# Kernel tuning notes

Measured on AMD Instinct MI355X. Metric: run time of the kernel, lower is better.

Reference implementation:

```python
import jax, jax.numpy as jnp
import numpy as np

ALPHA = 0.2  # LeakyReLU negative slope
NEG_INF = -9.0e15


def setup_inputs() -> dict:
    key = jax.random.key(0)
    k1, k2, k3, k4 = jax.random.split(key, 4)
    B, T, N, Fin, Fout = 2, 8, 2048, 64, 64
    h = jax.random.normal(k1, (B, T, N, Fin), dtype=jnp.float32)
    # xavier_uniform-like init for W [Fin,Fout] and a [2*Fout,1]
    limW = 1.414 * np.sqrt(6.0 / (Fin + Fout))
    W = jax.random.uniform(k2, (Fin, Fout), minval=-limW, maxval=limW, dtype=jnp.float32)
    lima = 1.414 * np.sqrt(6.0 / (2 * Fout + 1))
    a = jax.random.uniform(k3, (2 * Fout, 1), minval=-lima, maxval=lima, dtype=jnp.float32)
    adj = jax.random.randint(k4, (N, N), 0, 2).astype(jnp.int32)
    return {"h": h, "W": W, "a": a, "adj": adj}


def reference(h, W, a, adj):
    Fout = W.shape[1]
    Wh = jnp.matmul(h, W)                      # [B,T,N,Fout]
    Wh1 = jnp.matmul(Wh, a[:Fout])             # [B,T,N,1]
    Wh2 = jnp.matmul(Wh, a[Fout:])             # [B,T,N,1]
    e = Wh1 + jnp.swapaxes(Wh2, -1, -2)        # [B,T,N,N]
    e = jnp.where(e > 0, e, ALPHA * e)         # LeakyReLU
    e = jnp.where(adj > 0, e, jnp.float32(NEG_INF))  # adjacency mask
    # NOTE: source does F.softmax(dim=1) -> softmax over the T axis, replicated faithfully
    attention = jax.nn.softmax(e, axis=1)
    # dropout omitted (eval-mode reference)
    out = jnp.matmul(attention, Wh)            # [B,T,N,Fout]
    return jax.nn.elu(out)                     # concat=True
```

## Files before the change

### kernel.cpp

```cpp
#include <hip/hip_runtime.h>
#include <math.h>

#define B_ 2
#define T_ 8
#define N_ 2048
#define F_ 64
#define TI 32
#define JC 64
#define JCP 72
#define LOG2E 1.44269504088896f
#define PART_STRIDE ((size_t)B_ * T_ * N_ * F_)

typedef __attribute__((ext_vector_type(8))) short short8;
typedef __attribute__((ext_vector_type(4))) float f32x4;

__device__ __forceinline__ unsigned short f2bf(float x) {
  unsigned u = __float_as_uint(x);
  u += 0x7FFFu + ((u >> 16) & 1u);
  return (unsigned short)(u >> 16);
}

__device__ __forceinline__ unsigned cvt_pk_bf16(float lo, float hi) {
  unsigned r;
  asm("v_cvt_pk_bf16_f32 %0, %1, %2" : "=v"(r) : "v"(lo), "v"(hi));
  return r;
}

__global__ __launch_bounds__(256) void prep_kernel(
    const float* __restrict__ h, const float* __restrict__ W,
    const float* __restrict__ a, unsigned short* __restrict__ WhT,
    float* __restrict__ Wh1, float* __restrict__ Wh2) {
  __shared__ float Ws[64][64];
  __shared__ float hs[64][64];
  __shared__ float Whs[64][65];
  const int tid = threadIdx.x;
  const int row0 = blockIdx.x * 64;
  const int bt = row0 >> 11;
  const int j0 = row0 & 2047;
  for (int i = tid; i < 4096; i += 256) Ws[i >> 6][i & 63] = W[i];
  for (int i = tid; i < 4096; i += 256) hs[i >> 6][i & 63] = h[(size_t)row0 * 64 + i];
  __syncthreads();
  const int f = tid & 63;
  const int rq = tid >> 6;
  float acc[16];
#pragma unroll
  for (int m = 0; m < 16; ++m) acc[m] = 0.f;
#pragma unroll 4
  for (int k = 0; k < 64; ++k) {
    const float wvv = Ws[k][f];
#pragma unroll
    for (int m = 0; m < 16; ++m) acc[m] = fmaf(hs[rq * 16 + m][k], wvv, acc[m]);
  }
#pragma unroll
  for (int m = 0; m < 16; ++m) Whs[rq * 16 + m][f] = acc[m];
  __syncthreads();
  {
    const int r = tid >> 2, q = tid & 3;
    float s1 = 0.f, s2 = 0.f;
#pragma unroll
    for (int k = 0; k < 16; ++k) {
      const float v = Whs[r][q * 16 + k];
      s1 = fmaf(v, a[q * 16 + k], s1);
      s2 = fmaf(v, a[64 + q * 16 + k], s2);
    }
    s1 += __shfl_xor(s1, 1); s1 += __shfl_xor(s1, 2);
    s2 += __shfl_xor(s2, 1); s2 += __shfl_xor(s2, 2);
    if (q == 0) {
      Wh1[(size_t)bt * N_ + j0 + r] = s1 * LOG2E;
      Wh2[(size_t)bt * N_ + j0 + r] = s2 * LOG2E;
    }
  }
  {
    const int ff = tid & 63, cp = tid >> 6;
#pragma unroll
    for (int cc = 0; cc < 2; ++cc) {
      const int c = cp * 2 + cc;
      short8 v;
#pragma unroll
      for (int k = 0; k < 8; ++k) v[k] = (short)f2bf(Whs[c * 8 + k][ff]);
      *(short8*)(WhT + ((size_t)bt * 64 + ff) * N_ + j0 + c * 8) = v;
    }
  }
}

__global__ __launch_bounds__(512, 4) void gat_mfma(
    const unsigned short* __restrict__ WhT, const float* __restrict__ Wh1,
    const float* __restrict__ Wh2, const int* __restrict__ adj,
    float* __restrict__ out, float* __restrict__ parts, const int njq) {
  __shared__ unsigned short atts[2][T_][TI][JCP];
  __shared__ float wh2s[2][T_][JC];
  const int tid = threadIdx.x;
  const int jq = blockIdx.x % njq;
  const int rest = blockIdx.x / njq;
  const int i0 = (rest & 63) * TI;
  const int b = rest >> 6;
  const int jspan = N_ / njq;
  const int jbase = jq * jspan;
  const int nchunk = jspan / JC;

  const int wv = tid >> 6;
  const int lane = tid & 63;
  const int col = lane & 15;
  const int kg = lane >> 4;

  const int sii = tid >> 4;
  const int sjj = (tid & 15) * 4;
  const int st = tid >> 6, sj = tid & 63;

  const unsigned short* wtb = WhT + (size_t)(b * T_ + wv) * F_ * N_;
  const float* wh2b = Wh2 + (size_t)b * T_ * N_;
  const int* adjrow = adj + (size_t)(i0 + sii) * N_ + jbase;

  float w1r[T_];
#pragma unroll
  for (int t = 0; t < T_; ++t) w1r[t] = Wh1[(size_t)(b * T_ + t) * N_ + i0 + sii];

  f32x4 acc[2][4];
#pragma unroll
  for (int it = 0; it < 2; ++it)
#pragma unroll
    for (int nt = 0; nt < 4; ++nt) acc[it][nt] = {0.f, 0.f, 0.f, 0.f};

  wh2s[0][st][sj] = wh2b[(size_t)st * N_ + jbase + sj];
  int4 ad = *(const int4*)(adjrow + sjj);
  __syncthreads();

  for (int c = 0; c < nchunk; ++c) {
    const int j0 = jbase + c * JC;
    const int buf = c & 1;
    short8 breg[4][2];
#pragma unroll
    for (int nt = 0; nt < 4; ++nt)
#pragma unroll
      for (int ks = 0; ks < 2; ++ks)
        breg[nt][ks] = *(const short8*)(wtb + (size_t)(nt * 16 + col) * N_ +
                                        j0 + ks * 32 + kg * 8);
    if (c + 1 < nchunk)
      wh2s[buf ^ 1][st][sj] = wh2b[(size_t)st * N_ + j0 + JC + sj];
    int4 adn = ad;
    if (c + 1 < nchunk) adn = *(const int4*)(adjrow + (c + 1) * JC + sjj);

#pragma unroll
    for (int g = 0; g < 2; ++g) {
      const int c0 = sjj + 2 * g;
      const int a0i = g == 0 ? ad.x : ad.z;
      const int a1i = g == 0 ? ad.y : ad.w;
      float e0[T_], e1[T_];
      float s0 = 0.f, s1 = 0.f;
#pragma unroll
      for (int t = 0; t < T_; ++t) {
        const float2 w2 = *(const float2*)(&wh2s[buf][t][c0]);
        float x0 = w1r[t] + w2.x;
        float x1 = w1r[t] + w2.y;
        x0 = fmaxf(x0, 0.2f * x0);
        x1 = fmaxf(x1, 0.2f * x1);
        e0[t] = __builtin_amdgcn_exp2f(x0);
        e1[t] = __builtin_amdgcn_exp2f(x1);
        s0 += e0[t];
        s1 += e1[t];
      }
      const float r0 = a0i > 0 ? __builtin_amdgcn_rcpf(s0) : 0.f;
      const float r1 = a1i > 0 ? __builtin_amdgcn_rcpf(s1) : 0.f;
      const float d0 = a0i > 0 ? 0.f : 0.125f;
      const float d1 = a1i > 0 ? 0.f : 0.125f;
#pragma unroll
      for (int t = 0; t < T_; ++t) {
        const float av0 = fmaf(e0[t], r0, d0);
        const float av1 = fmaf(e1[t], r1, d1);
        *(unsigned*)&atts[buf][t][sii][c0] = cvt_pk_bf16(av0, av1);
      }
    }
    ad = adn;
    __syncthreads();
#pragma unroll
    for (int it = 0; it < 2; ++it) {
      const unsigned short* ab = &atts[buf][wv][it * 16 + col][kg * 8];
      const short8 a0 = *(const short8*)ab;
      const short8 a1 = *(const short8*)(ab + 32);
#pragma unroll
      for (int nt = 0; nt < 4; ++nt) {
        acc[it][nt] = __builtin_amdgcn_mfma_f32_16x16x32_bf16(a0, breg[nt][0], acc[it][nt], 0, 0, 0);
        acc[it][nt] = __builtin_amdgcn_mfma_f32_16x16x32_bf16(a1, breg[nt][1], acc[it][nt], 0, 0, 0);
      }
    }
  }

  float* dst = (jq == 0) ? out : (parts + (size_t)(jq - 1) * PART_STRIDE);
  float* ob = dst + ((size_t)(b * T_ + wv) * N_ + i0) * F_;
#pragma unroll
  for (int it = 0; it < 2; ++it) {
#pragma unroll
    for (int nt = 0; nt < 4; ++nt) {
#pragma unroll
      for (int r = 0; r < 4; ++r) {
        const int row = it * 16 + kg * 4 + r;
        ob[(size_t)row * F_ + nt * 16 + col] = acc[it][nt][r];
      }
    }
  }
}

__global__ __launch_bounds__(256) void combine_elu(
    float* __restrict__ out, const float* __restrict__ parts, const int nparts) {
  const size_t i = ((size_t)blockIdx.x * 256 + threadIdx.x) * 4;
  f32x4 o = *(const f32x4*)(out + i);
  for (int p = 0; p < nparts; ++p) {
    const f32x4 q = *(const f32x4*)(parts + p * PART_STRIDE + i);
#pragma unroll
    for (int k = 0; k < 4; ++k) o[k] += q[k];
  }
#pragma unroll
  for (int k = 0; k < 4; ++k) o[k] = o[k] > 0.f ? o[k] : expm1f(o[k]);
  *(f32x4*)(out + i) = o;
}

extern "C" void kernel_launch(void* const* d_in, const int* in_sizes, int n_in,
                              void* d_out, int out_size, void* d_ws, size_t ws_size,
                              hipStream_t stream) {
  const float* h   = (const float*)d_in[0];
  const float* W   = (const float*)d_in[1];
  const float* a   = (const float*)d_in[2];
  const int*   adj = (const int*)d_in[3];
  float* out = (float*)d_out;

  const size_t whtBytes = (size_t)B_ * T_ * F_ * N_ * 2;
  const size_t vBytes   = (size_t)B_ * T_ * N_ * 4;
  const size_t partB    = PART_STRIDE * 4;

  unsigned short* WhT = (unsigned short*)d_ws;
  float* Wh1   = (float*)((char*)d_ws + whtBytes);
  float* Wh2   = Wh1 + (size_t)B_ * T_ * N_;
  float* parts = Wh2 + (size_t)B_ * T_ * N_;

  const int njq = (ws_size >= whtBytes + 2 * vBytes + 3 * partB) ? 4
                : (ws_size >= whtBytes + 2 * vBytes + 1 * partB) ? 2 : 1;

  hipLaunchKernelGGL(prep_kernel, dim3(B_ * T_ * N_ / 64), dim3(256), 0, stream,
                     h, W, a, WhT, Wh1, Wh2);
  hipLaunchKernelGGL(gat_mfma, dim3(B_ * 64 * njq), dim3(512), 0, stream,
                     WhT, Wh1, Wh2, adj, out, parts, njq);
  if (njq > 1) {
    hipLaunchKernelGGL(combine_elu, dim3((unsigned)(PART_STRIDE / (256 * 4))), dim3(256),
                       0, stream, out, parts, njq - 1);
  } else {
    hipLaunchKernelGGL(combine_elu, dim3((unsigned)(PART_STRIDE / (256 * 4))), dim3(256),
                       0, stream, out, parts, 0);
  }
}
```

Measured before the change: 62.64 us.

## Store split-K partials in bf16, raise split to eight, add priority and lightweight barriers

The attention kernel now writes every split-K partial as bf16 into the workspace, and the combine kernel sums all partials and applies ELU with 8-wide vector loads. The split factor grows from 4 to 8 when the workspace allows, giving more blocks to fill the GPU. Barriers are replaced by an explicit lgkmcnt wait plus s_barrier, and the MFMA section runs at raised wave priority. The aim is to cut partial-sum write traffic and improve occupancy, at the cost of bf16 rounding in the partials, extra partial traffic from the larger split, and one more combine input per element.

```diff
diff --git a/kernel.cpp b/kernel.cpp
--- a/kernel.cpp
+++ b/kernel.cpp
@@ -25,6 +25,16 @@
   asm("v_cvt_pk_bf16_f32 %0, %1, %2" : "=v"(r) : "v"(lo), "v"(hi));
   return r;
 }
+
+__device__ __forceinline__ float bf2f(unsigned short u) {
+  return __uint_as_float(((unsigned)u) << 16);
+}
+
+#define BARRIER() do {                                      \
+    asm volatile("s_waitcnt lgkmcnt(0)" ::: "memory");      \
+    __builtin_amdgcn_s_barrier();                           \
+    __builtin_amdgcn_sched_barrier(0);                      \
+  } while (0)
 
 __global__ __launch_bounds__(256) void prep_kernel(
     const float* __restrict__ h, const float* __restrict__ W,
@@ -86,7 +96,7 @@
 __global__ __launch_bounds__(512, 4) void gat_mfma(
     const unsigned short* __restrict__ WhT, const float* __restrict__ Wh1,
     const float* __restrict__ Wh2, const int* __restrict__ adj,
-    float* __restrict__ out, float* __restrict__ parts, const int njq) {
+    unsigned short* __restrict__ parts, const int njq) {
   __shared__ unsigned short atts[2][T_][TI][JCP];
   __shared__ float wh2s[2][T_][JC];
   const int tid = threadIdx.x;
@@ -123,7 +133,7 @@
 
   wh2s[0][st][sj] = wh2b[(size_t)st * N_ + jbase + sj];
   int4 ad = *(const int4*)(adjrow + sjj);
-  __syncthreads();
+  BARRIER();
 
   for (int c = 0; c < nchunk; ++c) {
     const int j0 = jbase + c * JC;
@@ -171,7 +181,8 @@
       }
     }
     ad = adn;
-    __syncthreads();
+    BARRIER();
+    __builtin_amdgcn_s_setprio(1);
 #pragma unroll
     for (int it = 0; it < 2; ++it) {
       const unsigned short* ab = &atts[buf][wv][it * 16 + col][kg * 8];
@@ -183,10 +194,11 @@
         acc[it][nt] = __builtin_amdgcn_mfma_f32_16x16x32_bf16(a1, breg[nt][1], acc[it][nt], 0, 0, 0);
       }
     }
-  }
-
-  float* dst = (jq == 0) ? out : (parts + (size_t)(jq - 1) * PART_STRIDE);
-  float* ob = dst + ((size_t)(b * T_ + wv) * N_ + i0) * F_;
+    __builtin_amdgcn_s_setprio(0);
+  }
+
+  unsigned short* ob = parts + (size_t)jq * PART_STRIDE +
+                       ((size_t)(b * T_ + wv) * N_ + i0) * F_;
 #pragma unroll
   for (int it = 0; it < 2; ++it) {
 #pragma unroll
@@ -194,24 +206,31 @@
 #pragma unroll
       for (int r = 0; r < 4; ++r) {
         const int row = it * 16 + kg * 4 + r;
-        ob[(size_t)row * F_ + nt * 16 + col] = acc[it][nt][r];
+        const float x = acc[it][nt][r];
+        ob[(size_t)row * F_ + nt * 16 + col] = (unsigned short)cvt_pk_bf16(x, x);
       }
     }
   }
 }
 
 __global__ __launch_bounds__(256) void combine_elu(
-    float* __restrict__ out, const float* __restrict__ parts, const int nparts) {
-  const size_t i = ((size_t)blockIdx.x * 256 + threadIdx.x) * 4;
-  f32x4 o = *(const f32x4*)(out + i);
-  for (int p = 0; p < nparts; ++p) {
-    const f32x4 q = *(const f32x4*)(parts + p * PART_STRIDE + i);
-#pragma unroll
-    for (int k = 0; k < 4; ++k) o[k] += q[k];
-  }
-#pragma unroll
-  for (int k = 0; k < 4; ++k) o[k] = o[k] > 0.f ? o[k] : expm1f(o[k]);
-  *(f32x4*)(out + i) = o;
+    float* __restrict__ out, const unsigned short* __restrict__ parts,
+    const int njq) {
+  const size_t i = ((size_t)blockIdx.x * 256 + threadIdx.x) * 8;
+  float s[8] = {0.f, 0.f, 0.f, 0.f, 0.f, 0.f, 0.f, 0.f};
+  for (int p = 0; p < njq; ++p) {
+    const short8 v = *(const short8*)(parts + (size_t)p * PART_STRIDE + i);
+#pragma unroll
+    for (int k = 0; k < 8; ++k) s[k] += bf2f((unsigned short)v[k]);
+  }
+  f32x4 lo, hi;
+#pragma unroll
+  for (int k = 0; k < 4; ++k) {
+    lo[k] = s[k] > 0.f ? s[k] : expm1f(s[k]);
+    hi[k] = s[4 + k] > 0.f ? s[4 + k] : expm1f(s[4 + k]);
+  }
+  *(f32x4*)(out + i) = lo;
+  *(f32x4*)(out + i + 4) = hi;
 }
 
 extern "C" void kernel_launch(void* const* d_in, const int* in_sizes, int n_in,
@@ -225,25 +244,21 @@
 
   const size_t whtBytes = (size_t)B_ * T_ * F_ * N_ * 2;
   const size_t vBytes   = (size_t)B_ * T_ * N_ * 4;
-  const size_t partB    = PART_STRIDE * 4;
+  const size_t partB    = PART_STRIDE * 2;
 
   unsigned short* WhT = (unsigned short*)d_ws;
-  float* Wh1   = (float*)((char*)d_ws + whtBytes);
-  float* Wh2   = Wh1 + (size_t)B_ * T_ * N_;
-  float* parts = Wh2 + (size_t)B_ * T_ * N_;
-
-  const int njq = (ws_size >= whtBytes + 2 * vBytes + 3 * partB) ? 4
-                : (ws_size >= whtBytes + 2 * vBytes + 1 * partB) ? 2 : 1;
+  float* Wh1 = (float*)((char*)d_ws + whtBytes);
+  float* Wh2 = Wh1 + (size_t)B_ * T_ * N_;
+  unsigned short* parts = (unsigned short*)(Wh2 + (size_t)B_ * T_ * N_);
+
+  const size_t fixed = whtBytes + 2 * vBytes;
+  const int njq = (ws_size >= fixed + 8 * partB) ? 8
+                : (ws_size >= fixed + 2 * partB) ? 2 : 1;
 
   hipLaunchKernelGGL(prep_kernel, dim3(B_ * T_ * N_ / 64), dim3(256), 0, stream,
                      h, W, a, WhT, Wh1, Wh2);
-  hipLaunchKernelGGL(gat_mfma, dim3(B_ * 64 * njq), dim3(512), 0, stream,
-                     WhT, Wh1, Wh2, adj, out, parts, njq);
-  if (njq > 1) {
-    hipLaunchKernelGGL(combine_elu, dim3((unsigned)(PART_STRIDE / (256 * 4))), dim3(256),
-                       0, stream, out, parts, njq - 1);
-  } else {
-    hipLaunchKernelGGL(combine_elu, dim3((unsigned)(PART_STRIDE / (256 * 4))), dim3(256),
-                       0, stream, out, parts, 0);
-  }
-}
+  hipLaunchKernelGGL(gat_mfma, dim3(B_ * (N_ / TI) * njq), dim3(512), 0, stream,
+                     WhT, Wh1, Wh2, adj, parts, njq);
+  hipLaunchKernelGGL(combine_elu, dim3((unsigned)(PART_STRIDE / (256 * 8))), dim3(256),
+                     0, stream, out, parts, njq);
+}
```

New measurement: 66.05 us. 5.4% more time.
